# Performance work log

Hardware: AMD Instinct MI355X
Metric: run time of the kernel (lower is better)

Reference implementation:

```python
import jax, jax.numpy as jnp
import numpy as np

B, S, D, H, NH = 128, 512, 64, 256, 8
HD = H // NH
NEG = -10000000000.0


def _ln(x, g, b, eps=1e-5):
    m = x.mean(-1, keepdims=True)
    v = ((x - m) ** 2).mean(-1, keepdims=True)
    return (x - m) * jax.lax.rsqrt(v + eps) * g + b


def _mha(xq, xkv, mask, qW, qb, kW, kb, vW, vb, oW, ob):
    # mask: [B,1,1,S_kv] bool, True = masked out
    b, sq, _ = xq.shape
    sk = xkv.shape[1]
    Q = (xq @ qW + qb).reshape(b, sq, NH, HD).transpose(0, 2, 1, 3)
    K = (xkv @ kW + kb).reshape(b, sk, NH, HD).transpose(0, 2, 1, 3)
    V = (xkv @ vW + vb).reshape(b, sk, NH, HD).transpose(0, 2, 1, 3)
    energy = jnp.einsum('bhqd,bhkd->bhqk', Q, K) / jnp.sqrt(jnp.float32(HD))
    energy = jnp.where(mask, NEG, energy)
    attn = jax.nn.softmax(energy, axis=-1)  # dropout is identity in eval
    x = jnp.einsum('bhqk,bhkd->bhqd', attn, V)
    x = x.transpose(0, 2, 1, 3).reshape(b, sq, H)
    return x @ oW + ob


def _ffn(x, f1W, f1b, f2W, f2b):
    # NewGELU == tanh-approximate GELU (GPT-2)
    return jax.nn.gelu(x @ f1W + f1b, approximate=True) @ f2W + f2b


def _fwd(src, ln0sg, ln0sb, ln0tg, ln0tb, semW, semb, temW, temb,
         e_qW, e_qb, e_kW, e_kb, e_vW, e_vb, e_oW, e_ob, e_ln1g, e_ln1b,
         e_f1W, e_f1b, e_f2W, e_f2b, e_ln2g, e_ln2b,
         d_sqW, d_sqb, d_skW, d_skb, d_svW, d_svb, d_soW, d_sob, d_ln1g, d_ln1b,
         d_eqW, d_eqb, d_ekW, d_ekb, d_evW, d_evb, d_eoW, d_eob, d_ln2g, d_ln2b,
         d_f1W, d_f1b, d_f2W, d_f2b, d_ln3g, d_ln3b, outW, outb):
    valid = src.sum(-1) != 0                      # [B,S] (prod_fea == 0)
    amask = (~valid)[:, None, None, :]            # [B,1,1,S]; trg==src so trg_mask==src_mask
    embs_src = _ln(src, ln0sg, ln0sb) @ semW + semb   # emb_need
    embs_trg = _ln(src, ln0tg, ln0tb) @ temW + temb
    # encoder layer
    a = _mha(embs_src, embs_src, amask, e_qW, e_qb, e_kW, e_kb, e_vW, e_vb, e_oW, e_ob)
    x = _ln(embs_src + a, e_ln1g, e_ln1b)
    enc_src = _ln(x + _ffn(x, e_f1W, e_f1b, e_f2W, e_f2b), e_ln2g, e_ln2b)
    # decoder layer
    a = _mha(embs_trg, embs_trg, amask, d_sqW, d_sqb, d_skW, d_skb, d_svW, d_svb, d_soW, d_sob)
    t = _ln(embs_trg + a, d_ln1g, d_ln1b)
    a = _mha(t, enc_src, amask, d_eqW, d_eqb, d_ekW, d_ekb, d_evW, d_evb, d_eoW, d_eob)
    t = _ln(t + a, d_ln2g, d_ln2b)
    t = _ln(t + _ffn(t, d_f1W, d_f1b, d_f2W, d_f2b), d_ln3g, d_ln3b)
    logits = (t @ outW + outb)[..., 0]            # [B,S]
    p = jnp.exp(logits) * valid.astype(logits.dtype)
    return p / p.sum(-1, keepdims=True)           # multi_purchase=False branch


def setup_inputs() -> dict:
    key = jax.random.key(0)
    keys = iter(jax.random.split(key, 64))
    inp = {"src": jax.random.normal(next(keys), (B, S, D), dtype=jnp.float32)}

    def lin(name, i, o):
        inp[name + "W"] = jax.random.normal(next(keys), (i, o), dtype=jnp.float32) * 0.02
        inp[name + "b"] = jnp.zeros((o,), dtype=jnp.float32)

    def ln(name, d):
        inp[name + "g"] = jnp.ones((d,), dtype=jnp.float32)
        inp[name + "b"] = jnp.zeros((d,), dtype=jnp.float32)

    ln("ln0s", D); ln("ln0t", D)
    lin("sem", D, H); lin("tem", D, H)
    for n in ["e_q", "e_k", "e_v", "e_o"]:
        lin(n, H, H)
    ln("e_ln1", H); lin("e_f1", H, H); lin("e_f2", H, H); ln("e_ln2", H)
    for n in ["d_sq", "d_sk", "d_sv", "d_so", "d_eq", "d_ek", "d_ev", "d_eo"]:
        lin(n, H, H)
    ln("d_ln1", H); ln("d_ln2", H)
    lin("d_f1", H, H); lin("d_f2", H, H); ln("d_ln3", H)
    lin("out", H, 1)
    return inp


def reference(src, ln0sg, ln0sb, ln0tg, ln0tb, semW, semb, temW, temb,
              e_qW, e_qb, e_kW, e_kb, e_vW, e_vb, e_oW, e_ob, e_ln1g, e_ln1b,
              e_f1W, e_f1b, e_f2W, e_f2b, e_ln2g, e_ln2b,
              d_sqW, d_sqb, d_skW, d_skb, d_svW, d_svb, d_soW, d_sob, d_ln1g, d_ln1b,
              d_eqW, d_eqb, d_ekW, d_ekb, d_evW, d_evb, d_eoW, d_eob, d_ln2g, d_ln2b,
              d_f1W, d_f1b, d_f2W, d_f2b, d_ln3g, d_ln3b, outW, outb):
    return _fwd(src, ln0sg, ln0sb, ln0tg, ln0tb, semW, semb, temW, temb,
                e_qW, e_qb, e_kW, e_kb, e_vW, e_vb, e_oW, e_ob, e_ln1g, e_ln1b,
                e_f1W, e_f1b, e_f2W, e_f2b, e_ln2g, e_ln2b,
                d_sqW, d_sqb, d_skW, d_skb, d_svW, d_svb, d_soW, d_sob, d_ln1g, d_ln1b,
                d_eqW, d_eqb, d_ekW, d_ekb, d_evW, d_evb, d_eoW, d_eob, d_ln2g, d_ln2b,
                d_f1W, d_f1b, d_f2W, d_f2b, d_ln3g, d_ln3b, outW, outb)
```

## Files before the change

kernel.cpp:

```cpp
#include <hip/hip_runtime.h>
#include <hip/hip_bf16.h>


#define Bb  128
#define Ss  512
#define Hh  256
#define NHh 8
#define Mm  (Bb*Ss)

typedef unsigned short bf16_t;
typedef __attribute__((ext_vector_type(8))) short short8;
typedef __attribute__((ext_vector_type(4))) float f32x4;

__device__ __forceinline__ float bf2f(bf16_t h){
  union { unsigned int u; float f; } v; v.u = ((unsigned int)h)<<16; return v.f;
}
__device__ __forceinline__ bf16_t f2bf(float f){
  union { float f; unsigned int u; } v; v.f = f;
  unsigned int r = (v.u + 0x7fffu + ((v.u>>16)&1u)) >> 16;
  return (bf16_t)r;
}
__device__ __forceinline__ unsigned pk_bf16(float a, float b){
  union { __hip_bfloat162 h; unsigned u; } v;
  v.h = __float22bfloat162_rn(float2{a,b});
  return v.u;
}
__device__ __forceinline__ short8 ld_bf8(const bf16_t* p){
  union { uint4 u; short8 s; } v; v.u = *(const uint4*)p; return v.s;
}
__device__ __forceinline__ void gload16(const bf16_t* g, bf16_t* l){
  __builtin_amdgcn_global_load_lds(
      (const __attribute__((address_space(1))) void*)g,
      (__attribute__((address_space(3))) void*)l, 16, 0, 0);
}
__device__ __forceinline__ float exp2_hw(float x){
  float r; asm("v_exp_f32 %0, %1" : "=v"(r) : "v"(x)); return r;
}
__device__ __forceinline__ float gelu_f(float x){
  float u = 0.7978845608028654f*(x + 0.044715f*x*x*x);
  float e = __expf(2.0f*u);
  float th = 1.0f - 2.0f*__builtin_amdgcn_rcpf(e + 1.0f);
  return 0.5f*x*(1.0f + th);
}

struct PrepDesc { const float* s; unsigned off; int K; };
struct Prep18  { PrepDesc d[18]; };

__global__ __launch_bounds__(256) void k_prep(Prep18 p, bf16_t* __restrict__ arena)
{
  PrepDesc dd = p.d[blockIdx.y];
  int i = blockIdx.x*256 + threadIdx.x;
  if (i < dd.K*256){
    int k = i>>8, n = i&255;
    arena[dd.off + n*dd.K + k] = f2bf(dd.s[i]);
  }
}

__global__ __launch_bounds__(256) void k_ln0(const float* __restrict__ src,
    const float* __restrict__ gs, const float* __restrict__ bs,
    const float* __restrict__ gt, const float* __restrict__ bt,
    bf16_t* __restrict__ xs, bf16_t* __restrict__ xt, float* __restrict__ valid)
{
  int row  = blockIdx.x*4 + (threadIdx.x>>6);
  int lane = threadIdx.x & 63;
  float x = src[(size_t)row*64 + lane];
  float s = x;
  #pragma unroll
  for (int o=32;o>0;o>>=1) s += __shfl_xor(s,o);
  float mean = s*(1.0f/64.0f);
  float d = x - mean;
  float ss = d*d;
  #pragma unroll
  for (int o=32;o>0;o>>=1) ss += __shfl_xor(ss,o);
  float r = rsqrtf(ss*(1.0f/64.0f) + 1e-5f);
  float xn = d*r;
  xs[(size_t)row*64+lane] = f2bf(xn*gs[lane] + bs[lane]);
  xt[(size_t)row*64+lane] = f2bf(xn*gt[lane] + bt[lane]);
  if (lane==0) valid[row] = (s != 0.0f) ? 1.0f : 0.0f;
}

struct GemmJob  { const bf16_t* A; const bf16_t* Wt; const float* bias; bf16_t* C;
                  int outm; float cs; };
struct GemmJobs { GemmJob j[3]; };

template<int KK>
__global__ __launch_bounds__(256,4) void k_gemm3(GemmJobs jobs)
{
  __shared__ bf16_t As[8*512];
  __shared__ bf16_t Bs[32*512];
  GemmJob jb = jobs.j[blockIdx.y];
  int t = threadIdx.x, w = t>>6, lane = t&63, l15 = lane&15, quad = lane>>4;
  int m0 = blockIdx.x*64;
  f32x4 z = {0.f,0.f,0.f,0.f};
  f32x4 acc[4][4] = {{z,z,z,z},{z,z,z,z},{z,z,z,z},{z,z,z,z}};

  #pragma unroll
  for (int k0=0; k0<KK; k0+=64){
    #pragma unroll
    for (int j=0; j<2; j++){
      int id = 2*w + j; int kc32 = id>>2, mt = id&3;
      gload16(jb.A + (size_t)(m0 + mt*16 + l15)*KK + k0 + kc32*32 + quad*8,
              &As[id*512]);
    }
    #pragma unroll
    for (int j=0; j<8; j++){
      int id = 8*w + j; int kc32 = id>>4, gnt = id&15;
      gload16(jb.Wt + (size_t)(gnt*16 + l15)*KK + k0 + kc32*32 + quad*8,
              &Bs[id*512]);
    }
    __syncthreads();
    #pragma unroll
    for (int kc=0; kc<2; kc++){
      short8 a[4], b[4];
      #pragma unroll
      for (int mt=0; mt<4; mt++) a[mt] = ld_bf8(&As[(kc*4+mt)*512 + lane*8]);
      #pragma unroll
      for (int nt=0; nt<4; nt++) b[nt] = ld_bf8(&Bs[(kc*16 + w*4 + nt)*512 + lane*8]);
      #pragma unroll
      for (int mt=0; mt<4; mt++)
        #pragma unroll
        for (int nt=0; nt<4; nt++)
          acc[mt][nt] = __builtin_amdgcn_mfma_f32_16x16x32_bf16(a[mt], b[nt], acc[mt][nt], 0,0,0);
    }
    __syncthreads();
  }

  float bv[4];
  #pragma unroll
  for (int nt=0; nt<4; nt++) bv[nt] = jb.bias[w*64 + nt*16 + l15];
  float cs = jb.cs;

  if (jb.outm == 0){
    #pragma unroll
    for (int mt=0; mt<4; mt++)
      #pragma unroll
      for (int nt=0; nt<4; nt++){
        int m = m0 + mt*16 + quad*4;
        int col = w*64 + nt*16 + l15;
        #pragma unroll
        for (int r=0; r<4; r++)
          jb.C[(size_t)(m+r)*256 + col] = f2bf((acc[mt][nt][r] + bv[nt])*cs);
      }
  } else {
    #pragma unroll
    for (int mt=0; mt<4; mt++)
      #pragma unroll
      for (int nt=0; nt<4; nt++){
        int m = m0 + mt*16 + quad*4;
        int col = w*64 + nt*16 + l15;
        uint2 pk = { pk_bf16(acc[mt][nt][0]+bv[nt], acc[mt][nt][1]+bv[nt]),
                     pk_bf16(acc[mt][nt][2]+bv[nt], acc[mt][nt][3]+bv[nt]) };
        *(uint2*)&jb.C[((size_t)((m>>9)*256 + col))*512 + (m&511)] = pk;
      }
  }
}

struct QkvJob { const bf16_t* A;
                const bf16_t* Wt0; const bf16_t* Wt1; const bf16_t* Wt2;
                const float* b0; const float* b1; const float* b2;
                bf16_t* C0; bf16_t* C1; bf16_t* C2; float qs; };

__global__ __launch_bounds__(256,2) void k_qkv(QkvJob jb)
{
  __shared__ bf16_t As[32*512];
  __shared__ bf16_t Bs[32*512];
  int t = threadIdx.x, w = t>>6, lane = t&63, l15 = lane&15, quad = lane>>4;
  int m0 = blockIdx.x*64;
  f32x4 z = {0.f,0.f,0.f,0.f};

  #pragma unroll
  for (int j=0; j<8; j++){
    int id = 8*w + j; int kc32 = id>>2, mt = id&3;
    gload16(jb.A + (size_t)(m0 + mt*16 + l15)*256 + kc32*32 + quad*8,
            &As[id*512]);
  }

  const bf16_t* Wts[3]  = { jb.Wt0, jb.Wt1, jb.Wt2 };
  const float*  bias[3] = { jb.b0,  jb.b1,  jb.b2  };
  bf16_t*       Cs[3]   = { jb.C0,  jb.C1,  jb.C2  };

  #pragma unroll 1
  for (int o=0; o<3; o++){
    const bf16_t* Wt = Wts[o];
    f32x4 acc[4][4] = {{z,z,z,z},{z,z,z,z},{z,z,z,z},{z,z,z,z}};
    #pragma unroll 1
    for (int ki=0; ki<4; ki++){
      #pragma unroll
      for (int j=0; j<8; j++){
        int id = 8*w + j; int kc32 = id>>4, gnt = id&15;
        gload16(Wt + (size_t)(gnt*16 + l15)*256 + ki*64 + kc32*32 + quad*8,
                &Bs[id*512]);
      }
      __syncthreads();
      #pragma unroll
      for (int kc=0; kc<2; kc++){
        short8 a[4], b[4];
        #pragma unroll
        for (int mt=0; mt<4; mt++)
          a[mt] = ld_bf8(&As[((ki*2+kc)*4 + mt)*512 + lane*8]);
        #pragma unroll
        for (int nt=0; nt<4; nt++)
          b[nt] = ld_bf8(&Bs[(kc*16 + w*4 + nt)*512 + lane*8]);
        #pragma unroll
        for (int mt=0; mt<4; mt++)
          #pragma unroll
          for (int nt=0; nt<4; nt++)
            acc[mt][nt] = __builtin_amdgcn_mfma_f32_16x16x32_bf16(a[mt], b[nt], acc[mt][nt], 0,0,0);
      }
      __syncthreads();
    }
    float bv[4];
    #pragma unroll
    for (int nt=0; nt<4; nt++) bv[nt] = bias[o][w*64 + nt*16 + l15];
    bf16_t* C = Cs[o];
    if (o < 2){
      float cs = (o==0) ? jb.qs : 1.0f;
      #pragma unroll
      for (int mt=0; mt<4; mt++)
        #pragma unroll
        for (int nt=0; nt<4; nt++){
          int m = m0 + mt*16 + quad*4;
          int col = w*64 + nt*16 + l15;
          #pragma unroll
          for (int r=0; r<4; r++)
            C[(size_t)(m+r)*256 + col] = f2bf((acc[mt][nt][r] + bv[nt])*cs);
        }
    } else {
      #pragma unroll
      for (int mt=0; mt<4; mt++)
        #pragma unroll
        for (int nt=0; nt<4; nt++){
          int m = m0 + mt*16 + quad*4;
          int col = w*64 + nt*16 + l15;
          uint2 pk = { pk_bf16(acc[mt][nt][0]+bv[nt], acc[mt][nt][1]+bv[nt]),
                       pk_bf16(acc[mt][nt][2]+bv[nt], acc[mt][nt][3]+bv[nt]) };
          *(uint2*)&C[((size_t)((m>>9)*256 + col))*512 + (m&511)] = pk;
        }
    }
  }
}

template<int EPI, int OUTM, int KK>
__global__ __launch_bounds__(256,4) void k_gemm(const bf16_t* __restrict__ A,
    const bf16_t* __restrict__ Wt, const float* __restrict__ bias,
    void* __restrict__ Cv, const bf16_t* __restrict__ Pres,
    const float* __restrict__ g, const float* __restrict__ bb,
    const float* __restrict__ oW, const float* __restrict__ obp)
{
  __shared__ bf16_t As[8*512];
  __shared__ bf16_t Bs[32*512];
  int t = threadIdx.x, w = t>>6, lane = t&63, l15 = lane&15, quad = lane>>4;
  int m0 = blockIdx.x*64;
  f32x4 z = {0.f,0.f,0.f,0.f};
  f32x4 acc[4][4] = {{z,z,z,z},{z,z,z,z},{z,z,z,z},{z,z,z,z}};

  #pragma unroll
  for (int k0=0; k0<KK; k0+=64){
    #pragma unroll
    for (int j=0; j<2; j++){
      int id = 2*w + j; int kc32 = id>>2, mt = id&3;
      gload16(A + (size_t)(m0 + mt*16 + l15)*KK + k0 + kc32*32 + quad*8,
              &As[id*512]);
    }
    #pragma unroll
    for (int j=0; j<8; j++){
      int id = 8*w + j; int kc32 = id>>4, gnt = id&15;
      gload16(Wt + (size_t)(gnt*16 + l15)*KK + k0 + kc32*32 + quad*8,
              &Bs[id*512]);
    }
    __syncthreads();
    #pragma unroll
    for (int kc=0; kc<2; kc++){
      short8 a[4], b[4];
      #pragma unroll
      for (int mt=0; mt<4; mt++) a[mt] = ld_bf8(&As[(kc*4+mt)*512 + lane*8]);
      #pragma unroll
      for (int nt=0; nt<4; nt++) b[nt] = ld_bf8(&Bs[(kc*16 + w*4 + nt)*512 + lane*8]);
      #pragma unroll
      for (int mt=0; mt<4; mt++)
        #pragma unroll
        for (int nt=0; nt<4; nt++)
          acc[mt][nt] = __builtin_amdgcn_mfma_f32_16x16x32_bf16(a[mt], b[nt], acc[mt][nt], 0,0,0);
    }
    __syncthreads();
  }

  float bv[4];
  #pragma unroll
  for (int nt=0; nt<4; nt++) bv[nt] = bias[w*64 + nt*16 + l15];

  if (OUTM==0){
    #pragma unroll
    for (int mt=0; mt<4; mt++)
      #pragma unroll
      for (int nt=0; nt<4; nt++)
        #pragma unroll
        for (int r=0; r<4; r++){
          int row = m0 + mt*16 + quad*4 + r;
          int col = w*64 + nt*16 + l15;
          float v = acc[mt][nt][r] + bv[nt];
          if (EPI==1) v = gelu_f(v);
          ((bf16_t*)Cv)[(size_t)row*256 + col] = f2bf(v);
        }
  } else {
    float* RedS = (float*)As;
    float* RedQ = RedS + 256;
    #pragma unroll
    for (int mt=0; mt<4; mt++)
      #pragma unroll
      for (int r=0; r<4; r++){
        int row = m0 + mt*16 + quad*4 + r;
        const bf16_t* pr = Pres + (size_t)row*256;
        float s = 0.f, q = 0.f;
        #pragma unroll
        for (int nt=0; nt<4; nt++){
          float v = acc[mt][nt][r] + bv[nt] + bf2f(pr[w*64 + nt*16 + l15]);
          s += v; q += v*v;
        }
        s += __shfl_xor(s,1); s += __shfl_xor(s,2);
        s += __shfl_xor(s,4); s += __shfl_xor(s,8);
        q += __shfl_xor(q,1); q += __shfl_xor(q,2);
        q += __shfl_xor(q,4); q += __shfl_xor(q,8);
        if (l15==0){
          int rr = mt*16 + quad*4 + r;
          RedS[rr*4 + w] = s; RedQ[rr*4 + w] = q;
        }
      }
    __syncthreads();

    float gv[4], bbv[4], wv[4];
    #pragma unroll
    for (int nt=0; nt<4; nt++){ gv[nt] = g[w*64+nt*16+l15]; bbv[nt] = bb[w*64+nt*16+l15]; }
    if (OUTM==5)
      #pragma unroll
      for (int nt=0; nt<4; nt++) wv[nt] = oW[w*64+nt*16+l15];

    float s2p[4][4];
    #pragma unroll
    for (int mt=0; mt<4; mt++)
      #pragma unroll
      for (int r=0; r<4; r++){
        int rr = mt*16 + quad*4 + r;
        int row = m0 + rr;
        float S = RedS[rr*4+0]+RedS[rr*4+1]+RedS[rr*4+2]+RedS[rr*4+3];
        float Q = RedQ[rr*4+0]+RedQ[rr*4+1]+RedQ[rr*4+2]+RedQ[rr*4+3];
        float mean = S*(1.0f/256.0f);
        float var  = Q*(1.0f/256.0f) - mean*mean;
        float rstd = rsqrtf(var + 1e-5f);
        const bf16_t* pr = Pres + (size_t)row*256;
        if (OUTM==3){
          bf16_t* po = (bf16_t*)Cv + (size_t)row*256;
          #pragma unroll
          for (int nt=0; nt<4; nt++){
            float v = acc[mt][nt][r] + bv[nt] + bf2f(pr[w*64 + nt*16 + l15]);
            po[w*64 + nt*16 + l15] = f2bf((v-mean)*rstd*gv[nt] + bbv[nt]);
          }
        } else {
          float s2 = 0.f;
          #pragma unroll
          for (int nt=0; nt<4; nt++){
            float v = acc[mt][nt][r] + bv[nt] + bf2f(pr[w*64 + nt*16 + l15]);
            s2 += ((v-mean)*rstd*gv[nt] + bbv[nt]) * wv[nt];
          }
          s2 += __shfl_xor(s2,1); s2 += __shfl_xor(s2,2);
          s2 += __shfl_xor(s2,4); s2 += __shfl_xor(s2,8);
          s2p[mt][r] = s2;
        }
      }
    if (OUTM==5){
      __syncthreads();
      #pragma unroll
      for (int mt=0; mt<4; mt++)
        #pragma unroll
        for (int r=0; r<4; r++)
          if (l15==0) RedS[(mt*16 + quad*4 + r)*4 + w] = s2p[mt][r];
      __syncthreads();
      if (w==0){
        float S = RedS[lane*4+0]+RedS[lane*4+1]+RedS[lane*4+2]+RedS[lane*4+3];
        ((float*)Cv)[m0 + lane] = S + obp[0];
      }
    }
  }
}

__global__ __launch_bounds__(256) void k_attn(const bf16_t* __restrict__ Qm,
    const bf16_t* __restrict__ Km, const bf16_t* __restrict__ VT,
    const float* __restrict__ valid, bf16_t* __restrict__ AO)
{
  __shared__ bf16_t Pbuf[4][2][2][16][40];
  __shared__ float  Smask[512];
  int t = threadIdx.x, wave = t>>6, lane = t&63, l15 = lane&15, quad = lane>>4;
  int lid = blockIdx.x + 8*blockIdx.y + 1024*blockIdx.z;
  int hp = lid & 3, pb = (lid>>2)&1, g = (lid>>3)&7, bh = lid>>6;
  int h  = hp*2 + (g&1);
  int qc = g>>1;
  int b  = bh*2 + pb;
  int q0 = qc*128;

  Smask[t]     = (valid[b*Ss + t      ] != 0.f) ? 0.f : -1.44269504e10f;
  Smask[t+256] = (valid[b*Ss + t + 256] != 0.f) ? 0.f : -1.44269504e10f;
  __syncthreads();

  short8 aQ0 = ld_bf8(Qm + (size_t)(b*Ss + q0 + (wave*2  )*16 + l15)*256 + h*32 + quad*8);
  short8 aQ1 = ld_bf8(Qm + (size_t)(b*Ss + q0 + (wave*2+1)*16 + l15)*256 + h*32 + quad*8);
  const bf16_t* Kb = Km + (size_t)(b*Ss)*256 + h*32;
  const bf16_t* Vb = VT + ((size_t)b*256 + h*32)*512;

  f32x4 z = {0.f,0.f,0.f,0.f};
  f32x4 O0[2] = {z,z}, O1[2] = {z,z};
  float ls0 = 0.f, ls1 = 0.f;

  auto process = [&](int kt2n, short8 K0, short8 K1){
    int s = kt2n & 1;
    #pragma unroll
    for (int half=0; half<2; half++){
      short8 aK = half ? K1 : K0;
      int ktile = kt2n*2 + half;
      __builtin_amdgcn_s_setprio(1);
      f32x4 s0 = __builtin_amdgcn_mfma_f32_16x16x32_bf16(aK, aQ0, z, 0,0,0);
      f32x4 s1 = __builtin_amdgcn_mfma_f32_16x16x32_bf16(aK, aQ1, z, 0,0,0);
      __builtin_amdgcn_s_setprio(0);
      float4 mb = *(const float4*)&Smask[ktile*16 + quad*4];
      float p00 = exp2_hw(s0[0] + mb.x);
      float p01 = exp2_hw(s0[1] + mb.y);
      float p02 = exp2_hw(s0[2] + mb.z);
      float p03 = exp2_hw(s0[3] + mb.w);
      float p10 = exp2_hw(s1[0] + mb.x);
      float p11 = exp2_hw(s1[1] + mb.y);
      float p12 = exp2_hw(s1[2] + mb.z);
      float p13 = exp2_hw(s1[3] + mb.w);
      ls0 += (p00+p01)+(p02+p03);
      ls1 += (p10+p11)+(p12+p13);
      uint2 w0 = { pk_bf16(p00,p01), pk_bf16(p02,p03) };
      uint2 w1 = { pk_bf16(p10,p11), pk_bf16(p12,p13) };
      *(uint2*)&Pbuf[wave][0][s][l15][half*16 + quad*4] = w0;
      *(uint2*)&Pbuf[wave][1][s][l15][half*16 + quad*4] = w1;
    }
  };
  auto loadK = [&](int n, short8& K0, short8& K1){
    K0 = ld_bf8(Kb + (size_t)((n*2  )*16 + l15)*256 + quad*8);
    K1 = ld_bf8(Kb + (size_t)((n*2+1)*16 + l15)*256 + quad*8);
  };
  auto loadV = [&](int n, short8& V0, short8& V1){
    V0 = ld_bf8(Vb + (size_t)(l15   )*512 + n*32 + quad*8);
    V1 = ld_bf8(Vb + (size_t)(16+l15)*512 + n*32 + quad*8);
  };

  short8 cK0, cK1, pK0, pK1, nK0, nK1;
  short8 cV0, cV1, mV0, mV1, nV0, nV1;
  loadK(0, cK0, cK1);
  process(0, cK0, cK1);
  loadK(1, pK0, pK1);
  loadV(0, cV0, cV1);
  loadV(1, mV0, mV1);

  #pragma unroll 2
  for (int kt2=0; kt2<16; kt2++){
    if (kt2+2 < 16){ loadK(kt2+2, nK0, nK1); loadV(kt2+2, nV0, nV1); }
    int s = kt2 & 1;
    short8 aP0 = ld_bf8(&Pbuf[wave][0][s][l15][quad*8]);
    short8 aP1 = ld_bf8(&Pbuf[wave][1][s][l15][quad*8]);
    __builtin_amdgcn_s_setprio(1);
    O0[0] = __builtin_amdgcn_mfma_f32_16x16x32_bf16(aP0, cV0, O0[0], 0,0,0);
    O0[1] = __builtin_amdgcn_mfma_f32_16x16x32_bf16(aP0, cV1, O0[1], 0,0,0);
    O1[0] = __builtin_amdgcn_mfma_f32_16x16x32_bf16(aP1, cV0, O1[0], 0,0,0);
    O1[1] = __builtin_amdgcn_mfma_f32_16x16x32_bf16(aP1, cV1, O1[1], 0,0,0);
    __builtin_amdgcn_s_setprio(0);
    if (kt2+1 < 16) process(kt2+1, pK0, pK1);
    pK0 = nK0; pK1 = nK1;
    cV0 = mV0; cV1 = mV1; mV0 = nV0; mV1 = nV1;
  }

  ls0 += __shfl_xor(ls0,16); ls0 += __shfl_xor(ls0,32);
  ls1 += __shfl_xor(ls1,16); ls1 += __shfl_xor(ls1,32);
  float linv0 = (ls0 > 0.f) ? 1.0f/ls0 : 0.f;
  float linv1 = (ls1 > 0.f) ? 1.0f/ls1 : 0.f;
  float i0[4], i1[4];
  #pragma unroll
  for (int r=0; r<4; r++){
    i0[r] = __shfl(linv0, quad*4 + r);
    i1[r] = __shfl(linv1, quad*4 + r);
  }
  size_t r0 = (size_t)(b*Ss + q0 + (wave*2  )*16);
  size_t r1 = (size_t)(b*Ss + q0 + (wave*2+1)*16);
  #pragma unroll
  for (int nt=0; nt<2; nt++)
    #pragma unroll
    for (int r=0; r<4; r++){
      AO[(r0 + quad*4 + r)*256 + h*32 + nt*16 + l15] = f2bf(O0[nt][r]*i0[r]);
      AO[(r1 + quad*4 + r)*256 + h*32 + nt*16 + l15] = f2bf(O1[nt][r]*i1[r]);
    }
}

__global__ __launch_bounds__(256) void k_final(const float* __restrict__ L,
    const float* __restrict__ valid, float* __restrict__ out)
{
  __shared__ float wsum[4];
  int b = blockIdx.x, t = threadIdx.x;
  float e0 = __expf(L[b*Ss + t      ]) * valid[b*Ss + t      ];
  float e1 = __expf(L[b*Ss + 256 + t]) * valid[b*Ss + 256 + t];
  float s = e0 + e1;
  #pragma unroll
  for (int o=32;o>0;o>>=1) s += __shfl_xor(s,o);
  if ((t&63)==0) wsum[t>>6] = s;
  __syncthreads();
  float tot = wsum[0]+wsum[1]+wsum[2]+wsum[3];
  out[b*Ss + t      ] = e0/tot;
  out[b*Ss + 256 + t] = e1/tot;
}

extern "C" void kernel_launch(void* const* d_in, const int* in_sizes, int n_in,
                              void* d_out, int out_size, void* d_ws, size_t ws_size,
                              hipStream_t stream)
{
  #define F(i) ((const float*)d_in[(i)])
  bool sig = (in_sizes[33] == 256);
  const float* d_eqW  = F(sig?35:33); const float* d_eqb  = F(sig?36:34);
  const float* d_ekW  = F(sig?37:35); const float* d_ekb  = F(sig?38:36);
  const float* d_evW  = F(sig?39:37); const float* d_evb  = F(sig?40:38);
  const float* d_eoW  = F(sig?41:39); const float* d_eob  = F(sig?42:40);
  const float* d_ln1g = F(sig?33:41); const float* d_ln1b = F(sig?34:42);

  char* w = (char*)d_ws;
  bf16_t* P0 = (bf16_t*)w; w += (size_t)Mm*Hh*2;
  bf16_t* P1 = (bf16_t*)w; w += (size_t)Mm*Hh*2;
  bf16_t* H0 = (bf16_t*)w; w += (size_t)Mm*Hh*2;
  bf16_t* H1 = (bf16_t*)w;
  bf16_t* xs = (bf16_t*)w; w += (size_t)Mm*Hh*2;
  bf16_t* H2 = (bf16_t*)w;
  bf16_t* xt = (bf16_t*)w; w += (size_t)Mm*Hh*2;
  bf16_t* Wa = (bf16_t*)w; w += (size_t)(2*16384 + 16*65536)*2;
  float*  valid  = (float*)w; w += (size_t)Mm*4;
  float*  logits = (float*)w; w += (size_t)Mm*4;
  float* out = (float*)d_out;

  unsigned o_sem = 0, o_tem = 16384;
  unsigned o_w[16]; for (int i=0;i<16;i++) o_w[i] = 32768 + i*65536u;
  Prep18 pp;
  const float* srcs[18] = { F(5), F(7), F(9), F(11), F(13), F(15), F(19), F(21),
                            F(25), F(27), F(29), F(31), d_eqW, d_ekW, d_evW, d_eoW,
                            F(45), F(47) };
  unsigned offs[18] = { o_sem, o_tem, o_w[0],o_w[1],o_w[2],o_w[3],o_w[4],o_w[5],
                        o_w[6],o_w[7],o_w[8],o_w[9],o_w[10],o_w[11],o_w[12],o_w[13],
                        o_w[14],o_w[15] };
  for (int i=0;i<18;i++){ pp.d[i].s = srcs[i]; pp.d[i].off = offs[i]; pp.d[i].K = (i<2)?64:256; }

  dim3 blk(256);
  dim3 gLN(Mm/4);
  dim3 gG(Mm/64);
  dim3 gA(NHh, Bb, 4);
  dim3 gP(256, 18);
  const float* NF = nullptr; const bf16_t* NB = nullptr;
  const float QS = 0.17677669529663687f * 1.4426950408889634f;

  k_prep<<<gP, blk, 0, stream>>>(pp, Wa);
  k_ln0<<<gLN, blk, 0, stream>>>(F(0), F(1),F(2), F(3),F(4), xs, xt, valid);

  {
    GemmJobs js;
    js.j[0] = { xs, Wa+o_sem, F(6), P0, 0, 1.0f };
    js.j[1] = { xt, Wa+o_tem, F(8), P1, 0, 1.0f };
    js.j[2] = js.j[0];
    k_gemm3<64><<<dim3(Mm/64,2), blk, 0, stream>>>(js);
  }

  auto QJ = [&](const bf16_t* A, int wq, int wk, int wv,
                const float* bq, const float* bk, const float* bv2,
                const bf16_t* Ak){
    QkvJob j; j.A = A;
    j.Wt0 = Wa+o_w[wq]; j.Wt1 = Wa+o_w[wk]; j.Wt2 = Wa+o_w[wv];
    j.b0 = bq; j.b1 = bk; j.b2 = bv2;
    j.C0 = H0; j.C1 = H1; j.C2 = H2; j.qs = QS;
    (void)Ak; return j;
  };

  {
    QkvJob j = QJ(P0, 0,1,2, F(10),F(12),F(14), P0);
    k_qkv<<<gG, blk, 0, stream>>>(j);
  }
  k_attn<<<gA, blk, 0, stream>>>(H0, H1, H2, valid, H0);
  k_gemm<0,3,256><<<gG, blk, 0, stream>>>(H0, Wa+o_w[3], F(16), P0, P0, F(17),F(18), NF,NF);
  k_gemm<1,0,256><<<gG, blk, 0, stream>>>(P0, Wa+o_w[4], F(20), H0, NB,NF,NF,NF,NF);
  k_gemm<0,3,256><<<gG, blk, 0, stream>>>(H0, Wa+o_w[5], F(22), P0, P0, F(23),F(24), NF,NF);

  {
    QkvJob j = QJ(P1, 6,7,8, F(26),F(28),F(30), P1);
    k_qkv<<<gG, blk, 0, stream>>>(j);
  }
  k_attn<<<gA, blk, 0, stream>>>(H0, H1, H2, valid, H0);
  k_gemm<0,3,256><<<gG, blk, 0, stream>>>(H0, Wa+o_w[9], F(32), P1, P1, d_ln1g,d_ln1b, NF,NF);

  {
    k_gemm<0,0,256><<<gG, blk, 0, stream>>>(P1, Wa+o_w[10], d_eqb, H0, NB,NF,NF,NF,NF);
    GemmJobs js;
    js.j[0] = { P0, Wa+o_w[11], d_ekb, H1, 0, 1.0f };
    js.j[1] = { P0, Wa+o_w[12], d_evb, H2, 2, 1.0f };
    js.j[2] = js.j[0];
    k_gemm3<256><<<dim3(Mm/64,2), blk, 0, stream>>>(js);
  }
  k_attn<<<gA, blk, 0, stream>>>(H0, H1, H2, valid, H0);
  k_gemm<0,3,256><<<gG, blk, 0, stream>>>(H0, Wa+o_w[13], d_eob, P1, P1, F(43),F(44), NF,NF);

  k_gemm<1,0,256><<<gG, blk, 0, stream>>>(P1, Wa+o_w[14], F(46), H0, NB,NF,NF,NF,NF);
  k_gemm<0,5,256><<<gG, blk, 0, stream>>>(H0, Wa+o_w[15], F(48), logits, P1, F(49),F(50), F(51),F(52));

  k_final<<<dim3(Bb), blk, 0, stream>>>(logits, valid, out);
  #undef F
}
```

Baseline: 1.020 ms.

## Replace GEMMs with weight-stationary LDS kernel, full-row waves, no K-loop syncs

Adds k_wgemm, which loads the whole weight matrix (up to 256x256 bf16, 128KB) into LDS once per 512-thread block. Each wave then computes a 32x256 output tile, streaming A fragments straight from global memory into registers with one-step prefetch. Because a wave holds full rows, the LayerNorm epilogue needs no cross-wave LDS reduction or extra barriers. The fused QKV and multi-job GEMM kernels are split into separate launches, which adds launch count and rereads A. The large LDS footprint and 128 accumulator registers per lane limit occupancy, and the A global loads are not staged through LDS.

```diff
diff --git a/kernel.cpp b/kernel.cpp
--- a/kernel.cpp
+++ b/kernel.cpp
@@ -79,307 +79,124 @@
   if (lane==0) valid[row] = (s != 0.0f) ? 1.0f : 0.0f;
 }
 
-struct GemmJob  { const bf16_t* A; const bf16_t* Wt; const float* bias; bf16_t* C;
-                  int outm; float cs; };
-struct GemmJobs { GemmJob j[3]; };
-
-template<int KK>
-__global__ __launch_bounds__(256,4) void k_gemm3(GemmJobs jobs)
-{
-  __shared__ bf16_t As[8*512];
-  __shared__ bf16_t Bs[32*512];
-  GemmJob jb = jobs.j[blockIdx.y];
-  int t = threadIdx.x, w = t>>6, lane = t&63, l15 = lane&15, quad = lane>>4;
-  int m0 = blockIdx.x*64;
-  f32x4 z = {0.f,0.f,0.f,0.f};
-  f32x4 acc[4][4] = {{z,z,z,z},{z,z,z,z},{z,z,z,z},{z,z,z,z}};
-
-  #pragma unroll
-  for (int k0=0; k0<KK; k0+=64){
-    #pragma unroll
-    for (int j=0; j<2; j++){
-      int id = 2*w + j; int kc32 = id>>2, mt = id&3;
-      gload16(jb.A + (size_t)(m0 + mt*16 + l15)*KK + k0 + kc32*32 + quad*8,
-              &As[id*512]);
-    }
-    #pragma unroll
-    for (int j=0; j<8; j++){
-      int id = 8*w + j; int kc32 = id>>4, gnt = id&15;
-      gload16(jb.Wt + (size_t)(gnt*16 + l15)*KK + k0 + kc32*32 + quad*8,
-              &Bs[id*512]);
-    }
-    __syncthreads();
-    #pragma unroll
-    for (int kc=0; kc<2; kc++){
-      short8 a[4], b[4];
-      #pragma unroll
-      for (int mt=0; mt<4; mt++) a[mt] = ld_bf8(&As[(kc*4+mt)*512 + lane*8]);
-      #pragma unroll
-      for (int nt=0; nt<4; nt++) b[nt] = ld_bf8(&Bs[(kc*16 + w*4 + nt)*512 + lane*8]);
-      #pragma unroll
-      for (int mt=0; mt<4; mt++)
-        #pragma unroll
-        for (int nt=0; nt<4; nt++)
-          acc[mt][nt] = __builtin_amdgcn_mfma_f32_16x16x32_bf16(a[mt], b[nt], acc[mt][nt], 0,0,0);
-    }
-    __syncthreads();
-  }
-
-  float bv[4];
-  #pragma unroll
-  for (int nt=0; nt<4; nt++) bv[nt] = jb.bias[w*64 + nt*16 + l15];
-  float cs = jb.cs;
-
-  if (jb.outm == 0){
-    #pragma unroll
-    for (int mt=0; mt<4; mt++)
-      #pragma unroll
-      for (int nt=0; nt<4; nt++){
-        int m = m0 + mt*16 + quad*4;
-        int col = w*64 + nt*16 + l15;
-        #pragma unroll
-        for (int r=0; r<4; r++)
-          jb.C[(size_t)(m+r)*256 + col] = f2bf((acc[mt][nt][r] + bv[nt])*cs);
-      }
-  } else {
-    #pragma unroll
-    for (int mt=0; mt<4; mt++)
-      #pragma unroll
-      for (int nt=0; nt<4; nt++){
-        int m = m0 + mt*16 + quad*4;
-        int col = w*64 + nt*16 + l15;
-        uint2 pk = { pk_bf16(acc[mt][nt][0]+bv[nt], acc[mt][nt][1]+bv[nt]),
-                     pk_bf16(acc[mt][nt][2]+bv[nt], acc[mt][nt][3]+bv[nt]) };
-        *(uint2*)&jb.C[((size_t)((m>>9)*256 + col))*512 + (m&511)] = pk;
-      }
-  }
-}
-
-struct QkvJob { const bf16_t* A;
-                const bf16_t* Wt0; const bf16_t* Wt1; const bf16_t* Wt2;
-                const float* b0; const float* b1; const float* b2;
-                bf16_t* C0; bf16_t* C1; bf16_t* C2; float qs; };
-
-__global__ __launch_bounds__(256,2) void k_qkv(QkvJob jb)
-{
-  __shared__ bf16_t As[32*512];
-  __shared__ bf16_t Bs[32*512];
-  int t = threadIdx.x, w = t>>6, lane = t&63, l15 = lane&15, quad = lane>>4;
-  int m0 = blockIdx.x*64;
-  f32x4 z = {0.f,0.f,0.f,0.f};
-
-  #pragma unroll
-  for (int j=0; j<8; j++){
-    int id = 8*w + j; int kc32 = id>>2, mt = id&3;
-    gload16(jb.A + (size_t)(m0 + mt*16 + l15)*256 + kc32*32 + quad*8,
-            &As[id*512]);
-  }
-
-  const bf16_t* Wts[3]  = { jb.Wt0, jb.Wt1, jb.Wt2 };
-  const float*  bias[3] = { jb.b0,  jb.b1,  jb.b2  };
-  bf16_t*       Cs[3]   = { jb.C0,  jb.C1,  jb.C2  };
-
-  #pragma unroll 1
-  for (int o=0; o<3; o++){
-    const bf16_t* Wt = Wts[o];
-    f32x4 acc[4][4] = {{z,z,z,z},{z,z,z,z},{z,z,z,z},{z,z,z,z}};
-    #pragma unroll 1
-    for (int ki=0; ki<4; ki++){
-      #pragma unroll
-      for (int j=0; j<8; j++){
-        int id = 8*w + j; int kc32 = id>>4, gnt = id&15;
-        gload16(Wt + (size_t)(gnt*16 + l15)*256 + ki*64 + kc32*32 + quad*8,
-                &Bs[id*512]);
-      }
-      __syncthreads();
-      #pragma unroll
-      for (int kc=0; kc<2; kc++){
-        short8 a[4], b[4];
-        #pragma unroll
-        for (int mt=0; mt<4; mt++)
-          a[mt] = ld_bf8(&As[((ki*2+kc)*4 + mt)*512 + lane*8]);
-        #pragma unroll
-        for (int nt=0; nt<4; nt++)
-          b[nt] = ld_bf8(&Bs[(kc*16 + w*4 + nt)*512 + lane*8]);
-        #pragma unroll
-        for (int mt=0; mt<4; mt++)
-          #pragma unroll
-          for (int nt=0; nt<4; nt++)
-            acc[mt][nt] = __builtin_amdgcn_mfma_f32_16x16x32_bf16(a[mt], b[nt], acc[mt][nt], 0,0,0);
-      }
-      __syncthreads();
-    }
-    float bv[4];
-    #pragma unroll
-    for (int nt=0; nt<4; nt++) bv[nt] = bias[o][w*64 + nt*16 + l15];
-    bf16_t* C = Cs[o];
-    if (o < 2){
-      float cs = (o==0) ? jb.qs : 1.0f;
-      #pragma unroll
-      for (int mt=0; mt<4; mt++)
-        #pragma unroll
-        for (int nt=0; nt<4; nt++){
-          int m = m0 + mt*16 + quad*4;
-          int col = w*64 + nt*16 + l15;
-          #pragma unroll
-          for (int r=0; r<4; r++)
-            C[(size_t)(m+r)*256 + col] = f2bf((acc[mt][nt][r] + bv[nt])*cs);
-        }
-    } else {
-      #pragma unroll
-      for (int mt=0; mt<4; mt++)
-        #pragma unroll
-        for (int nt=0; nt<4; nt++){
-          int m = m0 + mt*16 + quad*4;
-          int col = w*64 + nt*16 + l15;
-          uint2 pk = { pk_bf16(acc[mt][nt][0]+bv[nt], acc[mt][nt][1]+bv[nt]),
-                       pk_bf16(acc[mt][nt][2]+bv[nt], acc[mt][nt][3]+bv[nt]) };
-          *(uint2*)&C[((size_t)((m>>9)*256 + col))*512 + (m&511)] = pk;
-        }
-    }
-  }
-}
-
 template<int EPI, int OUTM, int KK>
-__global__ __launch_bounds__(256,4) void k_gemm(const bf16_t* __restrict__ A,
+__global__ __launch_bounds__(512,2) void k_wgemm(const bf16_t* __restrict__ A,
     const bf16_t* __restrict__ Wt, const float* __restrict__ bias,
     void* __restrict__ Cv, const bf16_t* __restrict__ Pres,
     const float* __restrict__ g, const float* __restrict__ bb,
-    const float* __restrict__ oW, const float* __restrict__ obp)
-{
-  __shared__ bf16_t As[8*512];
-  __shared__ bf16_t Bs[32*512];
+    const float* __restrict__ oW, const float* __restrict__ obp, float cs)
+{
+  constexpr int NKC  = KK/32;
+  constexpr int IDS  = 16*NKC;
+  constexpr int PERW = IDS/8;
+  __shared__ bf16_t Ws[IDS*512];
+
   int t = threadIdx.x, w = t>>6, lane = t&63, l15 = lane&15, quad = lane>>4;
-  int m0 = blockIdx.x*64;
+  int r0 = blockIdx.x*256 + w*32;
+
+  #pragma unroll
+  for (int j=0; j<PERW; j++){
+    int id = w*PERW + j; int kc = id>>4, nt = id&15;
+    gload16(Wt + (size_t)(nt*16 + l15)*KK + kc*32 + quad*8, &Ws[id*512]);
+  }
+  short8 a0 = ld_bf8(A + (size_t)(r0      + l15)*KK + quad*8);
+  short8 a1 = ld_bf8(A + (size_t)(r0 + 16 + l15)*KK + quad*8);
+  __syncthreads();
+
   f32x4 z = {0.f,0.f,0.f,0.f};
-  f32x4 acc[4][4] = {{z,z,z,z},{z,z,z,z},{z,z,z,z},{z,z,z,z}};
-
-  #pragma unroll
-  for (int k0=0; k0<KK; k0+=64){
-    #pragma unroll
-    for (int j=0; j<2; j++){
-      int id = 2*w + j; int kc32 = id>>2, mt = id&3;
-      gload16(A + (size_t)(m0 + mt*16 + l15)*KK + k0 + kc32*32 + quad*8,
-              &As[id*512]);
+  f32x4 acc0[16], acc1[16];
+  #pragma unroll
+  for (int nt=0; nt<16; nt++){ acc0[nt] = z; acc1[nt] = z; }
+
+  #pragma unroll
+  for (int kc=0; kc<NKC; kc++){
+    short8 a0n, a1n;
+    if (kc+1 < NKC){
+      a0n = ld_bf8(A + (size_t)(r0      + l15)*KK + (kc+1)*32 + quad*8);
+      a1n = ld_bf8(A + (size_t)(r0 + 16 + l15)*KK + (kc+1)*32 + quad*8);
     }
     #pragma unroll
-    for (int j=0; j<8; j++){
-      int id = 8*w + j; int kc32 = id>>4, gnt = id&15;
-      gload16(Wt + (size_t)(gnt*16 + l15)*KK + k0 + kc32*32 + quad*8,
-              &Bs[id*512]);
+    for (int nt=0; nt<16; nt++){
+      short8 b = ld_bf8(&Ws[(kc*16 + nt)*512 + lane*8]);
+      acc0[nt] = __builtin_amdgcn_mfma_f32_16x16x32_bf16(a0, b, acc0[nt], 0,0,0);
+      acc1[nt] = __builtin_amdgcn_mfma_f32_16x16x32_bf16(a1, b, acc1[nt], 0,0,0);
     }
-    __syncthreads();
-    #pragma unroll
-    for (int kc=0; kc<2; kc++){
-      short8 a[4], b[4];
+    a0 = a0n; a1 = a1n;
+  }
+
+  float bv[16];
+  #pragma unroll
+  for (int nt=0; nt<16; nt++) bv[nt] = bias[nt*16 + l15];
+
+  if (OUTM==0){
+    auto epi = [&](f32x4 (&ac)[16], int tt){
+      int rowb = r0 + tt*16 + quad*4;
       #pragma unroll
-      for (int mt=0; mt<4; mt++) a[mt] = ld_bf8(&As[(kc*4+mt)*512 + lane*8]);
-      #pragma unroll
-      for (int nt=0; nt<4; nt++) b[nt] = ld_bf8(&Bs[(kc*16 + w*4 + nt)*512 + lane*8]);
-      #pragma unroll
-      for (int mt=0; mt<4; mt++)
-        #pragma unroll
-        for (int nt=0; nt<4; nt++)
-          acc[mt][nt] = __builtin_amdgcn_mfma_f32_16x16x32_bf16(a[mt], b[nt], acc[mt][nt], 0,0,0);
-    }
-    __syncthreads();
-  }
-
-  float bv[4];
-  #pragma unroll
-  for (int nt=0; nt<4; nt++) bv[nt] = bias[w*64 + nt*16 + l15];
-
-  if (OUTM==0){
-    #pragma unroll
-    for (int mt=0; mt<4; mt++)
-      #pragma unroll
-      for (int nt=0; nt<4; nt++)
+      for (int nt=0; nt<16; nt++)
         #pragma unroll
         for (int r=0; r<4; r++){
-          int row = m0 + mt*16 + quad*4 + r;
-          int col = w*64 + nt*16 + l15;
-          float v = acc[mt][nt][r] + bv[nt];
-          if (EPI==1) v = gelu_f(v);
-          ((bf16_t*)Cv)[(size_t)row*256 + col] = f2bf(v);
+          float v = ac[nt][r] + bv[nt];
+          v = (EPI==1) ? gelu_f(v) : v*cs;
+          ((bf16_t*)Cv)[(size_t)(rowb + r)*256 + nt*16 + l15] = f2bf(v);
         }
+    };
+    epi(acc0, 0); epi(acc1, 1);
+  } else if (OUTM==2){
+    auto epi = [&](f32x4 (&ac)[16], int tt){
+      int m = r0 + tt*16 + quad*4;
+      #pragma unroll
+      for (int nt=0; nt<16; nt++){
+        int col = nt*16 + l15;
+        uint2 pk = { pk_bf16(ac[nt][0]+bv[nt], ac[nt][1]+bv[nt]),
+                     pk_bf16(ac[nt][2]+bv[nt], ac[nt][3]+bv[nt]) };
+        *(uint2*)&((bf16_t*)Cv)[((size_t)((m>>9)*256 + col))*512 + (m&511)] = pk;
+      }
+    };
+    epi(acc0, 0); epi(acc1, 1);
   } else {
-    float* RedS = (float*)As;
-    float* RedQ = RedS + 256;
+    float gv[16], bbv[16], wv[16];
     #pragma unroll
-    for (int mt=0; mt<4; mt++)
+    for (int nt=0; nt<16; nt++){ gv[nt] = g[nt*16+l15]; bbv[nt] = bb[nt*16+l15]; }
+    if (OUTM==5)
+      #pragma unroll
+      for (int nt=0; nt<16; nt++) wv[nt] = oW[nt*16+l15];
+    float ob0 = (OUTM==5) ? obp[0] : 0.f;
+
+    auto epi = [&](f32x4 (&ac)[16], int tt){
       #pragma unroll
       for (int r=0; r<4; r++){
-        int row = m0 + mt*16 + quad*4 + r;
+        int row = r0 + tt*16 + quad*4 + r;
         const bf16_t* pr = Pres + (size_t)row*256;
-        float s = 0.f, q = 0.f;
+        float v[16]; float s = 0.f, q = 0.f;
         #pragma unroll
-        for (int nt=0; nt<4; nt++){
-          float v = acc[mt][nt][r] + bv[nt] + bf2f(pr[w*64 + nt*16 + l15]);
-          s += v; q += v*v;
+        for (int nt=0; nt<16; nt++){
+          v[nt] = ac[nt][r] + bv[nt] + bf2f(pr[nt*16 + l15]);
+          s += v[nt]; q += v[nt]*v[nt];
         }
         s += __shfl_xor(s,1); s += __shfl_xor(s,2);
         s += __shfl_xor(s,4); s += __shfl_xor(s,8);
         q += __shfl_xor(q,1); q += __shfl_xor(q,2);
         q += __shfl_xor(q,4); q += __shfl_xor(q,8);
-        if (l15==0){
-          int rr = mt*16 + quad*4 + r;
-          RedS[rr*4 + w] = s; RedQ[rr*4 + w] = q;
-        }
-      }
-    __syncthreads();
-
-    float gv[4], bbv[4], wv[4];
-    #pragma unroll
-    for (int nt=0; nt<4; nt++){ gv[nt] = g[w*64+nt*16+l15]; bbv[nt] = bb[w*64+nt*16+l15]; }
-    if (OUTM==5)
-      #pragma unroll
-      for (int nt=0; nt<4; nt++) wv[nt] = oW[w*64+nt*16+l15];
-
-    float s2p[4][4];
-    #pragma unroll
-    for (int mt=0; mt<4; mt++)
-      #pragma unroll
-      for (int r=0; r<4; r++){
-        int rr = mt*16 + quad*4 + r;
-        int row = m0 + rr;
-        float S = RedS[rr*4+0]+RedS[rr*4+1]+RedS[rr*4+2]+RedS[rr*4+3];
-        float Q = RedQ[rr*4+0]+RedQ[rr*4+1]+RedQ[rr*4+2]+RedQ[rr*4+3];
-        float mean = S*(1.0f/256.0f);
-        float var  = Q*(1.0f/256.0f) - mean*mean;
+        float mean = s*(1.0f/256.0f);
+        float var  = q*(1.0f/256.0f) - mean*mean;
         float rstd = rsqrtf(var + 1e-5f);
-        const bf16_t* pr = Pres + (size_t)row*256;
         if (OUTM==3){
           bf16_t* po = (bf16_t*)Cv + (size_t)row*256;
           #pragma unroll
-          for (int nt=0; nt<4; nt++){
-            float v = acc[mt][nt][r] + bv[nt] + bf2f(pr[w*64 + nt*16 + l15]);
-            po[w*64 + nt*16 + l15] = f2bf((v-mean)*rstd*gv[nt] + bbv[nt]);
-          }
+          for (int nt=0; nt<16; nt++)
+            po[nt*16 + l15] = f2bf((v[nt]-mean)*rstd*gv[nt] + bbv[nt]);
         } else {
           float s2 = 0.f;
           #pragma unroll
-          for (int nt=0; nt<4; nt++){
-            float v = acc[mt][nt][r] + bv[nt] + bf2f(pr[w*64 + nt*16 + l15]);
-            s2 += ((v-mean)*rstd*gv[nt] + bbv[nt]) * wv[nt];
-          }
+          for (int nt=0; nt<16; nt++)
+            s2 += ((v[nt]-mean)*rstd*gv[nt] + bbv[nt]) * wv[nt];
           s2 += __shfl_xor(s2,1); s2 += __shfl_xor(s2,2);
           s2 += __shfl_xor(s2,4); s2 += __shfl_xor(s2,8);
-          s2p[mt][r] = s2;
+          if (l15==0) ((float*)Cv)[row] = s2 + ob0;
         }
       }
-    if (OUTM==5){
-      __syncthreads();
-      #pragma unroll
-      for (int mt=0; mt<4; mt++)
-        #pragma unroll
-        for (int r=0; r<4; r++)
-          if (l15==0) RedS[(mt*16 + quad*4 + r)*4 + w] = s2p[mt][r];
-      __syncthreads();
-      if (w==0){
-        float S = RedS[lane*4+0]+RedS[lane*4+1]+RedS[lane*4+2]+RedS[lane*4+3];
-        ((float*)Cv)[m0 + lane] = S + obp[0];
-      }
-    }
+    };
+    epi(acc0, 0); epi(acc1, 1);
   }
 }
 
@@ -546,8 +363,9 @@
   for (int i=0;i<18;i++){ pp.d[i].s = srcs[i]; pp.d[i].off = offs[i]; pp.d[i].K = (i<2)?64:256; }
 
   dim3 blk(256);
+  dim3 blk512(512);
   dim3 gLN(Mm/4);
-  dim3 gG(Mm/64);
+  dim3 gW(256);
   dim3 gA(NHh, Bb, 4);
   dim3 gP(256, 18);
   const float* NF = nullptr; const bf16_t* NB = nullptr;
@@ -556,53 +374,31 @@
   k_prep<<<gP, blk, 0, stream>>>(pp, Wa);
   k_ln0<<<gLN, blk, 0, stream>>>(F(0), F(1),F(2), F(3),F(4), xs, xt, valid);
 
-  {
-    GemmJobs js;
-    js.j[0] = { xs, Wa+o_sem, F(6), P0, 0, 1.0f };
-    js.j[1] = { xt, Wa+o_tem, F(8), P1, 0, 1.0f };
-    js.j[2] = js.j[0];
-    k_gemm3<64><<<dim3(Mm/64,2), blk, 0, stream>>>(js);
-  }
-
-  auto QJ = [&](const bf16_t* A, int wq, int wk, int wv,
-                const float* bq, const float* bk, const float* bv2,
-                const bf16_t* Ak){
-    QkvJob j; j.A = A;
-    j.Wt0 = Wa+o_w[wq]; j.Wt1 = Wa+o_w[wk]; j.Wt2 = Wa+o_w[wv];
-    j.b0 = bq; j.b1 = bk; j.b2 = bv2;
-    j.C0 = H0; j.C1 = H1; j.C2 = H2; j.qs = QS;
-    (void)Ak; return j;
-  };
-
-  {
-    QkvJob j = QJ(P0, 0,1,2, F(10),F(12),F(14), P0);
-    k_qkv<<<gG, blk, 0, stream>>>(j);
-  }
+  k_wgemm<0,0,64><<<gW, blk512, 0, stream>>>(xs, Wa+o_sem, F(6), P0, NB, NF,NF,NF,NF, 1.0f);
+  k_wgemm<0,0,64><<<gW, blk512, 0, stream>>>(xt, Wa+o_tem, F(8), P1, NB, NF,NF,NF,NF, 1.0f);
+
+  k_wgemm<0,0,256><<<gW, blk512, 0, stream>>>(P0, Wa+o_w[0], F(10), H0, NB, NF,NF,NF,NF, QS);
+  k_wgemm<0,0,256><<<gW, blk512, 0, stream>>>(P0, Wa+o_w[1], F(12), H1, NB, NF,NF,NF,NF, 1.0f);
+  k_wgemm<0,2,256><<<gW, blk512, 0, stream>>>(P0, Wa+o_w[2], F(14), H2, NB, NF,NF,NF,NF, 1.0f);
   k_attn<<<gA, blk, 0, stream>>>(H0, H1, H2, valid, H0);
-  k_gemm<0,3,256><<<gG, blk, 0, stream>>>(H0, Wa+o_w[3], F(16), P0, P0, F(17),F(18), NF,NF);
-  k_gemm<1,0,256><<<gG, blk, 0, stream>>>(P0, Wa+o_w[4], F(20), H0, NB,NF,NF,NF,NF);
-  k_gemm<0,3,256><<<gG, blk, 0, stream>>>(H0, Wa+o_w[5], F(22), P0, P0, F(23),F(24), NF,NF);
-
-  {
-    QkvJob j = QJ(P1, 6,7,8, F(26),F(28),F(30), P1);
-    k_qkv<<<gG, blk, 0, stream>>>(j);
-  }
+  k_wgemm<0,3,256><<<gW, blk512, 0, stream>>>(H0, Wa+o_w[3], F(16), P0, P0, F(17),F(18), NF,NF, 1.0f);
+  k_wgemm<1,0,256><<<gW, blk512, 0, stream>>>(P0, Wa+o_w[4], F(20), H0, NB, NF,NF,NF,NF, 1.0f);
+  k_wgemm<0,3,256><<<gW, blk512, 0, stream>>>(H0, Wa+o_w[5], F(22), P0, P0, F(23),F(24), NF,NF, 1.0f);
+
+  k_wgemm<0,0,256><<<gW, blk512, 0, stream>>>(P1, Wa+o_w[6], F(26), H0, NB, NF,NF,NF,NF, QS);
+  k_wgemm<0,0,256><<<gW, blk512, 0, stream>>>(P1, Wa+o_w[7], F(28), H1, NB, NF,NF,NF,NF, 1.0f);
+  k_wgemm<0,2,256><<<gW, blk512, 0, stream>>>(P1, Wa+o_w[8], F(30), H2, NB, NF,NF,NF,NF, 1.0f);
   k_attn<<<gA, blk, 0, stream>>>(H0, H1, H2, valid, H0);
-  k_gemm<0,3,256><<<gG, blk, 0, stream>>>(H0, Wa+o_w[9], F(32), P1, P1, d_ln1g,d_ln1b, NF,NF);
-
-  {
-    k_gemm<0,0,256><<<gG, blk, 0, stream>>>(P1, Wa+o_w[10], d_eqb, H0, NB,NF,NF,NF,NF);
-    GemmJobs js;
-    js.j[0] = { P0, Wa+o_w[11], d_ekb, H1, 0, 1.0f };
-    js.j[1] = { P0, Wa+o_w[12], d_evb, H2, 2, 1.0f };
-    js.j[2] = js.j[0];
-    k_gemm3<256><<<dim3(Mm/64,2), blk, 0, stream>>>(js);
-  }
+  k_wgemm<0,3,256><<<gW, blk512, 0, stream>>>(H0, Wa+o_w[9], F(32), P1, P1, d_ln1g,d_ln1b, NF,NF, 1.0f);
+
+  k_wgemm<0,0,256><<<gW, blk512, 0, stream>>>(P1, Wa+o_w[10], d_eqb, H0, NB, NF,NF,NF,NF, QS);
+  k_wgemm<0,0,256><<<gW, blk512, 0, stream>>>(P0, Wa+o_w[11], d_ekb, H1, NB, NF,NF,NF,NF, 1.0f);
+  k_wgemm<0,2,256><<<gW, blk512, 0, stream>>>(P0, Wa+o_w[12], d_evb, H2, NB, NF,NF,NF,NF, 1.0f);
   k_attn<<<gA, blk, 0, stream>>>(H0, H1, H2, valid, H0);
-  k_gemm<0,3,256><<<gG, blk, 0, stream>>>(H0, Wa+o_w[13], d_eob, P1, P1, F(43),F(44), NF,NF);
-
-  k_gemm<1,0,256><<<gG, blk, 0, stream>>>(P1, Wa+o_w[14], F(46), H0, NB,NF,NF,NF,NF);
-  k_gemm<0,5,256><<<gG, blk, 0, stream>>>(H0, Wa+o_w[15], F(48), logits, P1, F(49),F(50), F(51),F(52));
+  k_wgemm<0,3,256><<<gW, blk512, 0, stream>>>(H0, Wa+o_w[13], d_eob, P1, P1, F(43),F(44), NF,NF, 1.0f);
+
+  k_wgemm<1,0,256><<<gW, blk512, 0, stream>>>(P1, Wa+o_w[14], F(46), H0, NB, NF,NF,NF,NF, 1.0f);
+  k_wgemm<0,5,256><<<gW, blk512, 0, stream>>>(H0, Wa+o_w[15], F(48), logits, P1, F(49),F(50), F(51),F(52), 1.0f);
 
   k_final<<<dim3(Bb), blk, 0, stream>>>(logits, valid, out);
   #undef F
```

Result: faster. 929.2 us (median of 2 runs) (-8.9%).
